# Kernel optimization log

Measured on AMD Instinct MI355X. Metric: run time of the kernel, lower is better.

The kernel has to match this reference:

```python
import jax, jax.numpy as jnp
import numpy as np

N, F_IN, F_HID, F_OUT = 16384, 128, 128, 64
EDGE_P = 0.001  # Bernoulli edge probability -> avg degree ~16


def _sage_conv(x, mask_t, deg_inv, Wl, b, Wr):
    # PyG SAGEConv (mean aggr): out = lin_l(mean_agg) + lin_r(x); lin_l has bias.
    agg = (mask_t @ x) * deg_inv[:, None]  # [N, Fin] mean over incoming edges
    return agg @ Wl.T + b + x @ Wr.T


def setup_inputs() -> dict:
    key = jax.random.key(0)
    ks = jax.random.split(key, 12)
    x = jax.random.normal(ks[0], (N, F_IN), dtype=jnp.float32)
    adj = (jax.random.uniform(ks[1], (N, N)) < EDGE_P).astype(jnp.float32)

    def lin(k, fo, fi):
        s = 1.0 / np.sqrt(fi)
        return jax.random.uniform(k, (fo, fi), jnp.float32, -s, s)

    dims = [(F_HID, F_IN), (F_HID, F_HID), (F_OUT, F_HID)]
    params = {}
    for i, (fo, fi) in enumerate(dims):
        params[f"Wl{i}"] = lin(ks[2 + 3 * i], fo, fi)
        params[f"b{i}"] = jnp.zeros((fo,), jnp.float32)
        params[f"Wr{i}"] = lin(ks[3 + 3 * i], fo, fi)
    return {"x": x, "adj": adj, **params}


def reference(x, adj, Wl0, b0, Wr0, Wl1, b1, Wr1, Wl2, b2, Wr2):
    # edge (r, c): adj[r, c] != 0, source r -> target c (PyG convention).
    mask = (adj != 0).astype(x.dtype)
    deg = mask.sum(axis=0)                      # incoming degree per target node
    deg_inv = jnp.where(deg > 0, 1.0 / jnp.maximum(deg, 1.0), 0.0)
    mask_t = mask.T                             # [target, source]
    # Dropout layers are identity in eval mode.
    h = jax.nn.relu(_sage_conv(x, mask_t, deg_inv, Wl0, b0, Wr0))
    h = jax.nn.relu(_sage_conv(h, mask_t, deg_inv, Wl1, b1, Wr1))
    out = _sage_conv(h, mask_t, deg_inv, Wl2, b2, Wr2)
    return out
```

## Files before the change

### kernel.cpp

```cpp
#include <hip/hip_runtime.h>


#define NN 16384
#define SLOTC 64

typedef int iv4 __attribute__((ext_vector_type(4)));

#define OFF_DEG   0u
#define OFF_SLOT  65536u
#define OFF_WT0   (65536u + 4194304u)
#define OFF_WT1   (OFF_WT0 + 131072u)
#define OFF_WT2   (OFF_WT1 + 131072u)
#define OFF_H1    (OFF_WT2 + 65536u)
#define OFF_H2    (OFF_H1 + 4u * NN * 128u)

__global__ void k_wt(const float* __restrict__ Wl0, const float* __restrict__ Wr0,
                     const float* __restrict__ Wl1, const float* __restrict__ Wr1,
                     const float* __restrict__ Wl2, const float* __restrict__ Wr2,
                     float* __restrict__ wt0, float* __restrict__ wt1,
                     float* __restrict__ wt2, int* __restrict__ deg) {
    int g = blockIdx.x * 256 + threadIdx.x;
    if (g < NN) deg[g] = 0;
    if (g < 32768) {
        int k = g >> 7, o = g & 127;
        wt0[g] = (k < 128) ? Wl0[o * 128 + k] : Wr0[o * 128 + (k - 128)];
    } else if (g < 65536) {
        int gg = g - 32768;
        int k = gg >> 7, o = gg & 127;
        wt1[gg] = (k < 128) ? Wl1[o * 128 + k] : Wr1[o * 128 + (k - 128)];
    } else if (g < 81920) {
        int gg = g - 65536;
        int k = gg >> 6, o = gg & 63;
        wt2[gg] = (k < 128) ? Wl2[o * 128 + k] : Wr2[o * 128 + (k - 128)];
    }
}

__device__ __forceinline__ void emit_hits(iv4 v, int idx4, int* __restrict__ deg,
                                          int* __restrict__ slots) {
    if ((v.x | v.y | v.z | v.w) == 0) return;
    int base = idx4 << 2;
    int s = base >> 14;
    int t = base & (NN - 1);
    int w[4] = {v.x, v.y, v.z, v.w};
    #pragma unroll
    for (int k = 0; k < 4; ++k) {
        if (w[k] != 0) {
            int pos = atomicAdd(&deg[t + k], 1);
            if (pos < SLOTC) slots[(t + k) * SLOTC + pos] = s;
        }
    }
}

__global__ __launch_bounds__(256) void k_count(
    const iv4* __restrict__ adj4, int* __restrict__ deg,
    int* __restrict__ slots) {
    const int stride = 2048 * 256;
    int i = blockIdx.x * 256 + threadIdx.x;
    iv4 a = __builtin_nontemporal_load(&adj4[i]);
    iv4 b = __builtin_nontemporal_load(&adj4[i + stride]);
    #pragma unroll 1
    for (int n = 0; n < 63; ++n) {
        iv4 c = __builtin_nontemporal_load(&adj4[i + 2 * stride]);
        iv4 d = __builtin_nontemporal_load(&adj4[i + 3 * stride]);
        emit_hits(a, i, deg, slots);
        emit_hits(b, i + stride, deg, slots);
        a = c; b = d; i += 2 * stride;
    }
    emit_hits(a, i, deg, slots);
    emit_hits(b, i + stride, deg, slots);
}

template <int FOUT, bool RELU>
__global__ __launch_bounds__(256) void k_layer(
    const float4* __restrict__ hin,
    float* __restrict__ hout,
    const int* __restrict__ slots, const int* __restrict__ deg,
    const float4* __restrict__ Wt4,
    const float* __restrict__ bias)
{
    constexpr int S4 = 66;
    __shared__ float4 z[32 * S4];
    const int tid = threadIdx.x;
    const int nodeBase = blockIdx.x * 32;

    #pragma unroll
    for (int r = 0; r < 4; ++r) {
        int g = tid + 256 * r;
        int n = g >> 5, j = g & 31;
        z[n * S4 + 32 + j] = hin[(nodeBase + n) * 32 + j];
    }

    {
        const int nl = tid >> 3;
        const int q = tid & 7;
        const int node = nodeBase + nl;
        const int d = deg[node];
        const int dc = d < SLOTC ? d : SLOTC;
        const int* el = slots + node * SLOTC;
        float4 acc[4];
        #pragma unroll
        for (int k = 0; k < 4; ++k) acc[k] = make_float4(0.f, 0.f, 0.f, 0.f);
        int e = 0;
        for (; e + 4 <= dc; e += 4) {
            int4 s4 = *(const int4*)(el + e);
            const float4* r0 = hin + s4.x * 32;
            const float4* r1 = hin + s4.y * 32;
            const float4* r2 = hin + s4.z * 32;
            const float4* r3 = hin + s4.w * 32;
            #pragma unroll
            for (int k = 0; k < 4; ++k) {
                float4 v0 = r0[q + 8 * k];
                float4 v1 = r1[q + 8 * k];
                float4 v2 = r2[q + 8 * k];
                float4 v3 = r3[q + 8 * k];
                acc[k].x += (v0.x + v1.x) + (v2.x + v3.x);
                acc[k].y += (v0.y + v1.y) + (v2.y + v3.y);
                acc[k].z += (v0.z + v1.z) + (v2.z + v3.z);
                acc[k].w += (v0.w + v1.w) + (v2.w + v3.w);
            }
        }
        for (; e < dc; ++e) {
            const float4* r0 = hin + el[e] * 32;
            #pragma unroll
            for (int k = 0; k < 4; ++k) {
                float4 va = r0[q + 8 * k];
                acc[k].x += va.x; acc[k].y += va.y;
                acc[k].z += va.z; acc[k].w += va.w;
            }
        }
        const float di = d > 0 ? 1.0f / (float)d : 0.0f;
        #pragma unroll
        for (int k = 0; k < 4; ++k) {
            acc[k].x *= di; acc[k].y *= di; acc[k].z *= di; acc[k].w *= di;
            z[nl * S4 + q + 8 * k] = acc[k];
        }
    }
    __syncthreads();

    constexpr int TO = FOUT / 4;
    constexpr int TN = 256 / TO;
    constexpr int NPT = 32 / TN;
    const int to = tid % TO;
    const int tn = tid / TO;

    float4 acc[NPT];
    #pragma unroll
    for (int m = 0; m < NPT; ++m) acc[m] = make_float4(0.f, 0.f, 0.f, 0.f);

    #pragma unroll 2
    for (int k4 = 0; k4 < 64; ++k4) {
        float4 w0 = Wt4[(4 * k4 + 0) * TO + to];
        float4 w1 = Wt4[(4 * k4 + 1) * TO + to];
        float4 w2 = Wt4[(4 * k4 + 2) * TO + to];
        float4 w3 = Wt4[(4 * k4 + 3) * TO + to];
        #pragma unroll
        for (int m = 0; m < NPT; ++m) {
            float4 a = z[(tn * NPT + m) * S4 + k4];
            acc[m].x += a.x * w0.x + a.y * w1.x + a.z * w2.x + a.w * w3.x;
            acc[m].y += a.x * w0.y + a.y * w1.y + a.z * w2.y + a.w * w3.y;
            acc[m].z += a.x * w0.z + a.y * w1.z + a.z * w2.z + a.w * w3.z;
            acc[m].w += a.x * w0.w + a.y * w1.w + a.z * w2.w + a.w * w3.w;
        }
    }

    const float4 bb = ((const float4*)bias)[to];
    #pragma unroll
    for (int m = 0; m < NPT; ++m) {
        float4 o;
        o.x = acc[m].x + bb.x; o.y = acc[m].y + bb.y;
        o.z = acc[m].z + bb.z; o.w = acc[m].w + bb.w;
        if (RELU) {
            o.x = fmaxf(o.x, 0.f); o.y = fmaxf(o.y, 0.f);
            o.z = fmaxf(o.z, 0.f); o.w = fmaxf(o.w, 0.f);
        }
        ((float4*)hout)[(nodeBase + tn * NPT + m) * TO + to] = o;
    }
}

extern "C" void kernel_launch(void* const* d_in, const int* in_sizes, int n_in,
                              void* d_out, int out_size, void* d_ws, size_t ws_size,
                              hipStream_t stream) {
    const float* x = (const float*)d_in[0];
    const iv4* adj4 = (const iv4*)d_in[1];
    const float* Wl0 = (const float*)d_in[2];
    const float* b0 = (const float*)d_in[3];
    const float* Wr0 = (const float*)d_in[4];
    const float* Wl1 = (const float*)d_in[5];
    const float* b1 = (const float*)d_in[6];
    const float* Wr1 = (const float*)d_in[7];
    const float* Wl2 = (const float*)d_in[8];
    const float* b2 = (const float*)d_in[9];
    const float* Wr2 = (const float*)d_in[10];

    char* ws = (char*)d_ws;
    int* deg = (int*)(ws + OFF_DEG);
    int* slots = (int*)(ws + OFF_SLOT);
    float* wt0 = (float*)(ws + OFF_WT0);
    float* wt1 = (float*)(ws + OFF_WT1);
    float* wt2 = (float*)(ws + OFF_WT2);
    float* h1 = (float*)(ws + OFF_H1);
    float* h2 = (float*)(ws + OFF_H2);

    k_wt<<<320, 256, 0, stream>>>(Wl0, Wr0, Wl1, Wr1, Wl2, Wr2,
                                  wt0, wt1, wt2, deg);
    k_count<<<2048, 256, 0, stream>>>(adj4, deg, slots);
    k_layer<128, true><<<NN / 32, 256, 0, stream>>>(
        (const float4*)x, h1, slots, deg, (const float4*)wt0, b0);
    k_layer<128, true><<<NN / 32, 256, 0, stream>>>(
        (const float4*)h1, h2, slots, deg, (const float4*)wt1, b1);
    k_layer<64, false><<<NN / 32, 256, 0, stream>>>(
        (const float4*)h2, (float*)d_out, slots, deg, (const float4*)wt2, b2);
}
```

Baseline: 1.411 ms.

## Buffer adjacency hits per thread and fill CSR slots in a separate pass

The dense adjacency scan no longer does atomics inline. Each thread stores up to 8 hit (source, target) pairs in a private buffer, and a new k_fill kernel then does the degree atomics and slot writes, so atomic latency is taken off the bandwidth-bound scan. Separately, the layer kernels now process 16 nodes per block instead of 32, with 16 lanes per node during gather, which doubles the block count and raises occupancy. The cost is an extra kernel launch and extra global traffic for the hit buffer, and the weight reuse per block is halved.

Result: slower. 1.513 ms (+7.2%).

```diff
diff --git a/kernel.cpp b/kernel.cpp
--- a/kernel.cpp
+++ b/kernel.cpp
@@ -3,6 +3,7 @@
 
 #define NN 16384
 #define SLOTC 64
+#define HCAP 8
 
 typedef int iv4 __attribute__((ext_vector_type(4)));
 
@@ -13,6 +14,8 @@
 #define OFF_WT2   (OFF_WT1 + 131072u)
 #define OFF_H1    (OFF_WT2 + 65536u)
 #define OFF_H2    (OFF_H1 + 4u * NN * 128u)
+#define OFF_HCNT  (OFF_H2 + 4u * NN * 128u)
+#define OFF_HBUF  (OFF_HCNT + 524288u)
 
 __global__ void k_wt(const float* __restrict__ Wl0, const float* __restrict__ Wr0,
                      const float* __restrict__ Wl1, const float* __restrict__ Wr1,
@@ -35,39 +38,67 @@
     }
 }
 
-__device__ __forceinline__ void emit_hits(iv4 v, int idx4, int* __restrict__ deg,
+__device__ __forceinline__ void scan_emit(iv4 v, int idx4, unsigned int hbase,
+                                          int& cnt, unsigned int* __restrict__ hbuf,
+                                          int* __restrict__ deg,
                                           int* __restrict__ slots) {
     if ((v.x | v.y | v.z | v.w) == 0) return;
-    int base = idx4 << 2;
-    int s = base >> 14;
-    int t = base & (NN - 1);
+    int fb = idx4 << 2;
+    int s = fb >> 14;
+    int t = fb & (NN - 1);
     int w[4] = {v.x, v.y, v.z, v.w};
     #pragma unroll
     for (int k = 0; k < 4; ++k) {
         if (w[k] != 0) {
-            int pos = atomicAdd(&deg[t + k], 1);
-            if (pos < SLOTC) slots[(t + k) * SLOTC + pos] = s;
-        }
-    }
-}
-
-__global__ __launch_bounds__(256) void k_count(
+            if (cnt < HCAP) {
+                hbuf[hbase + (unsigned int)cnt] =
+                    ((unsigned int)s << 14) | (unsigned int)(t + k);
+            } else {
+                int pos = atomicAdd(&deg[t + k], 1);
+                if (pos < SLOTC) slots[(t + k) * SLOTC + pos] = s;
+            }
+            ++cnt;
+        }
+    }
+}
+
+__global__ __launch_bounds__(256) void k_scan(
     const iv4* __restrict__ adj4, int* __restrict__ deg,
-    int* __restrict__ slots) {
+    int* __restrict__ slots, unsigned int* __restrict__ hbuf,
+    unsigned char* __restrict__ hcnt) {
     const int stride = 2048 * 256;
-    int i = blockIdx.x * 256 + threadIdx.x;
+    const int g0 = blockIdx.x * 256 + threadIdx.x;
+    const unsigned int hbase = ((unsigned int)g0) << 3;
+    int cnt = 0;
+    int i = g0;
     iv4 a = __builtin_nontemporal_load(&adj4[i]);
     iv4 b = __builtin_nontemporal_load(&adj4[i + stride]);
     #pragma unroll 1
     for (int n = 0; n < 63; ++n) {
         iv4 c = __builtin_nontemporal_load(&adj4[i + 2 * stride]);
         iv4 d = __builtin_nontemporal_load(&adj4[i + 3 * stride]);
-        emit_hits(a, i, deg, slots);
-        emit_hits(b, i + stride, deg, slots);
+        scan_emit(a, i, hbase, cnt, hbuf, deg, slots);
+        scan_emit(b, i + stride, hbase, cnt, hbuf, deg, slots);
         a = c; b = d; i += 2 * stride;
     }
-    emit_hits(a, i, deg, slots);
-    emit_hits(b, i + stride, deg, slots);
+    scan_emit(a, i, hbase, cnt, hbuf, deg, slots);
+    scan_emit(b, i + stride, hbase, cnt, hbuf, deg, slots);
+    hcnt[g0] = (unsigned char)(cnt > HCAP ? HCAP : cnt);
+}
+
+__global__ __launch_bounds__(256) void k_fill(
+    const unsigned int* __restrict__ hbuf, const unsigned char* __restrict__ hcnt,
+    int* __restrict__ deg, int* __restrict__ slots) {
+    int g = blockIdx.x * 256 + threadIdx.x;
+    int cnt = hcnt[g];
+    unsigned int hbase = ((unsigned int)g) << 3;
+    for (int j = 0; j < cnt; ++j) {
+        unsigned int v = hbuf[hbase + (unsigned int)j];
+        int s = (int)(v >> 14);
+        int t = (int)(v & (NN - 1));
+        int pos = atomicAdd(&deg[t], 1);
+        if (pos < SLOTC) slots[t * SLOTC + pos] = s;
+    }
 }
 
 template <int FOUT, bool RELU>
@@ -79,27 +110,26 @@
     const float* __restrict__ bias)
 {
     constexpr int S4 = 66;
-    __shared__ float4 z[32 * S4];
+    __shared__ float4 z[16 * S4];
     const int tid = threadIdx.x;
-    const int nodeBase = blockIdx.x * 32;
-
-    #pragma unroll
-    for (int r = 0; r < 4; ++r) {
+    const int nodeBase = blockIdx.x * 16;
+
+    #pragma unroll
+    for (int r = 0; r < 2; ++r) {
         int g = tid + 256 * r;
         int n = g >> 5, j = g & 31;
         z[n * S4 + 32 + j] = hin[(nodeBase + n) * 32 + j];
     }
 
     {
-        const int nl = tid >> 3;
-        const int q = tid & 7;
+        const int nl = tid >> 4;
+        const int q = tid & 15;
         const int node = nodeBase + nl;
         const int d = deg[node];
         const int dc = d < SLOTC ? d : SLOTC;
         const int* el = slots + node * SLOTC;
-        float4 acc[4];
-        #pragma unroll
-        for (int k = 0; k < 4; ++k) acc[k] = make_float4(0.f, 0.f, 0.f, 0.f);
+        float4 acc0 = make_float4(0.f, 0.f, 0.f, 0.f);
+        float4 acc1 = make_float4(0.f, 0.f, 0.f, 0.f);
         int e = 0;
         for (; e + 4 <= dc; e += 4) {
             int4 s4 = *(const int4*)(el + e);
@@ -107,39 +137,34 @@
             const float4* r1 = hin + s4.y * 32;
             const float4* r2 = hin + s4.z * 32;
             const float4* r3 = hin + s4.w * 32;
-            #pragma unroll
-            for (int k = 0; k < 4; ++k) {
-                float4 v0 = r0[q + 8 * k];
-                float4 v1 = r1[q + 8 * k];
-                float4 v2 = r2[q + 8 * k];
-                float4 v3 = r3[q + 8 * k];
-                acc[k].x += (v0.x + v1.x) + (v2.x + v3.x);
-                acc[k].y += (v0.y + v1.y) + (v2.y + v3.y);
-                acc[k].z += (v0.z + v1.z) + (v2.z + v3.z);
-                acc[k].w += (v0.w + v1.w) + (v2.w + v3.w);
-            }
+            float4 v0 = r0[q],      v1 = r1[q],      v2 = r2[q],      v3 = r3[q];
+            float4 u0 = r0[q + 16], u1 = r1[q + 16], u2 = r2[q + 16], u3 = r3[q + 16];
+            acc0.x += (v0.x + v1.x) + (v2.x + v3.x);
+            acc0.y += (v0.y + v1.y) + (v2.y + v3.y);
+            acc0.z += (v0.z + v1.z) + (v2.z + v3.z);
+            acc0.w += (v0.w + v1.w) + (v2.w + v3.w);
+            acc1.x += (u0.x + u1.x) + (u2.x + u3.x);
+            acc1.y += (u0.y + u1.y) + (u2.y + u3.y);
+            acc1.z += (u0.z + u1.z) + (u2.z + u3.z);
+            acc1.w += (u0.w + u1.w) + (u2.w + u3.w);
         }
         for (; e < dc; ++e) {
             const float4* r0 = hin + el[e] * 32;
-            #pragma unroll
-            for (int k = 0; k < 4; ++k) {
-                float4 va = r0[q + 8 * k];
-                acc[k].x += va.x; acc[k].y += va.y;
-                acc[k].z += va.z; acc[k].w += va.w;
-            }
+            float4 va = r0[q], ua = r0[q + 16];
+            acc0.x += va.x; acc0.y += va.y; acc0.z += va.z; acc0.w += va.w;
+            acc1.x += ua.x; acc1.y += ua.y; acc1.z += ua.z; acc1.w += ua.w;
         }
         const float di = d > 0 ? 1.0f / (float)d : 0.0f;
-        #pragma unroll
-        for (int k = 0; k < 4; ++k) {
-            acc[k].x *= di; acc[k].y *= di; acc[k].z *= di; acc[k].w *= di;
-            z[nl * S4 + q + 8 * k] = acc[k];
-        }
+        acc0.x *= di; acc0.y *= di; acc0.z *= di; acc0.w *= di;
+        acc1.x *= di; acc1.y *= di; acc1.z *= di; acc1.w *= di;
+        z[nl * S4 + q] = acc0;
+        z[nl * S4 + q + 16] = acc1;
     }
     __syncthreads();
 
     constexpr int TO = FOUT / 4;
     constexpr int TN = 256 / TO;
-    constexpr int NPT = 32 / TN;
+    constexpr int NPT = 16 / TN;
     const int to = tid % TO;
     const int tn = tid / TO;
 
@@ -200,14 +225,17 @@
     float* wt2 = (float*)(ws + OFF_WT2);
     float* h1 = (float*)(ws + OFF_H1);
     float* h2 = (float*)(ws + OFF_H2);
+    unsigned char* hcnt = (unsigned char*)(ws + OFF_HCNT);
+    unsigned int* hbuf = (unsigned int*)(ws + OFF_HBUF);
 
     k_wt<<<320, 256, 0, stream>>>(Wl0, Wr0, Wl1, Wr1, Wl2, Wr2,
                                   wt0, wt1, wt2, deg);
-    k_count<<<2048, 256, 0, stream>>>(adj4, deg, slots);
-    k_layer<128, true><<<NN / 32, 256, 0, stream>>>(
+    k_scan<<<2048, 256, 0, stream>>>(adj4, deg, slots, hbuf, hcnt);
+    k_fill<<<2048, 256, 0, stream>>>(hbuf, hcnt, deg, slots);
+    k_layer<128, true><<<NN / 16, 256, 0, stream>>>(
         (const float4*)x, h1, slots, deg, (const float4*)wt0, b0);
-    k_layer<128, true><<<NN / 32, 256, 0, stream>>>(
+    k_layer<128, true><<<NN / 16, 256, 0, stream>>>(
         (const float4*)h1, h2, slots, deg, (const float4*)wt1, b1);
-    k_layer<64, false><<<NN / 32, 256, 0, stream>>>(
+    k_layer<64, false><<<NN / 16, 256, 0, stream>>>(
         (const float4*)h2, (float*)d_out, slots, deg, (const float4*)wt2, b2);
 }
```
